# Optimization experiments

Measured on AMD Instinct MI355X. Metric: run time of the kernel, lower is better.

Reference implementation:

```python
import jax, jax.numpy as jnp
import numpy as np

H_DIM = 4096
N_HEADS = 4
D_HEAD = H_DIM // N_HEADS  # 1024; also forced to equal the node count N
N = D_HEAD
LN_EPS = 1e-5


def setup_inputs() -> dict:
    key = jax.random.key(0)
    ks = jax.random.split(key, 10)
    s = 0.02
    return {
        "node1": jax.random.normal(ks[0], (N, H_DIM), dtype=jnp.float32),
        "node2": jax.random.normal(ks[1], (N, H_DIM), dtype=jnp.float32),
        # stacked per-head projection weights (torch Linear y = x @ W^T + b; here W stored as [h, in, out])
        "Wq": jax.random.normal(ks[2], (N_HEADS, H_DIM, D_HEAD), dtype=jnp.float32) * s,
        "bq": jax.random.normal(ks[3], (N_HEADS, D_HEAD), dtype=jnp.float32) * s,
        "Wk": jax.random.normal(ks[4], (N_HEADS, H_DIM, D_HEAD), dtype=jnp.float32) * s,
        "bk": jax.random.normal(ks[5], (N_HEADS, D_HEAD), dtype=jnp.float32) * s,
        "Wv": jax.random.normal(ks[6], (N_HEADS, H_DIM, D_HEAD), dtype=jnp.float32) * s,
        "bv": jax.random.normal(ks[7], (N_HEADS, D_HEAD), dtype=jnp.float32) * s,
        "gamma": jnp.ones((H_DIM,), dtype=jnp.float32),
        "beta": jnp.zeros((H_DIM,), dtype=jnp.float32),
    }


def reference(node1, node2, Wq, bq, Wk, bk, Wv, bv, gamma, beta):
    # per-head projections: [h, N, d]
    q = jnp.einsum('nd,hdf->hnf', node1, Wq) + bq[:, None, :]
    k = jnp.einsum('md,hdf->hmf', node2, Wk) + bk[:, None, :]
    v = jnp.einsum('md,hdf->hmf', node2, Wv) + bv[:, None, :]
    scale = 1.0 / jnp.sqrt(jnp.asarray(D_HEAD, dtype=q.dtype))
    # scores [h, N, N]; elementwise-multiplied by v (no softmax). Valid because N == D_HEAD.
    r = (jnp.einsum('hnf,hmf->hnm', q, k) * scale) * v
    # concat heads along last dim: [N, h * d] = [N, H_DIM]
    out = jnp.transpose(r, (1, 0, 2)).reshape(N, H_DIM)
    # LayerNorm over last dim (biased variance, matching torch)
    mu = jnp.mean(out, axis=-1, keepdims=True)
    var = jnp.mean((out - mu) ** 2, axis=-1, keepdims=True)
    return (out - mu) * jax.lax.rsqrt(var + LN_EPS) * gamma + beta
```

## Files before the change

kernel.cpp:

```cpp
#include <hip/hip_runtime.h>

#define H_DIM 4096
#define DH 1024
#define NROWS 1024

typedef __attribute__((ext_vector_type(8))) short short8;
typedef __attribute__((ext_vector_type(4))) short short4v;
typedef __attribute__((ext_vector_type(4))) float f32x4;

#define AS_GLOBAL __attribute__((address_space(1)))
#define AS_LDS __attribute__((address_space(3)))

__device__ __forceinline__ short f2bf(float f) {
  union { float f; unsigned u; } v; v.f = f;
  unsigned r = v.u + 0x7fffu + ((v.u >> 16) & 1u);
  return (short)(r >> 16);
}
__device__ __forceinline__ float bf2f(short s) {
  union { unsigned u; float f; } v;
  v.u = ((unsigned)(unsigned short)s) << 16;
  return v.f;
}

__device__ __forceinline__ void gload16(const void* g, void* l) {
  __builtin_amdgcn_global_load_lds((const AS_GLOBAL void*)g, (AS_LDS void*)l, 16, 0, 0);
}

__global__ void convert_nodes(const float* __restrict__ n1, const float* __restrict__ n2,
                              short* __restrict__ o1, short* __restrict__ o2) {
  const float* src = blockIdx.y ? n2 : n1;
  short* dst = blockIdx.y ? o2 : o1;
  const size_t i = ((size_t)blockIdx.x * 256 + threadIdx.x) * 8;
  f32x4 a = *(const f32x4*)&src[i];
  f32x4 b = *(const f32x4*)&src[i + 4];
  short8 s;
  s[0] = f2bf(a.x); s[1] = f2bf(a.y); s[2] = f2bf(a.z); s[3] = f2bf(a.w);
  s[4] = f2bf(b.x); s[5] = f2bf(b.y); s[6] = f2bf(b.z); s[7] = f2bf(b.w);
  *(short8*)&dst[i] = s;
}

__global__ void convert_w_all(const float* __restrict__ Wq, const float* __restrict__ Wk,
                              const float* __restrict__ Wv, short* __restrict__ Wt) {
  __shared__ short tile[64][72];
  const int z = blockIdx.z, dt = blockIdx.y, ft = blockIdx.x;
  const float* W = (z < 4) ? Wq : (z < 8) ? Wk : Wv;
  const int h = z & 3;
  const float* Wh = W + (size_t)h * H_DIM * DH;
  short* Wth = Wt + (size_t)z * DH * H_DIM;
  const int t = threadIdx.x;
  {
    const int d = t >> 2, f0 = (t & 3) * 16;
    const float* src = Wh + (size_t)(dt * 64 + d) * DH + ft * 64 + f0;
    f32x4 v0 = *(const f32x4*)(src + 0);
    f32x4 v1 = *(const f32x4*)(src + 4);
    f32x4 v2 = *(const f32x4*)(src + 8);
    f32x4 v3 = *(const f32x4*)(src + 12);
    short8 s0, s1;
    s0[0] = f2bf(v0.x); s0[1] = f2bf(v0.y); s0[2] = f2bf(v0.z); s0[3] = f2bf(v0.w);
    s0[4] = f2bf(v1.x); s0[5] = f2bf(v1.y); s0[6] = f2bf(v1.z); s0[7] = f2bf(v1.w);
    s1[0] = f2bf(v2.x); s1[1] = f2bf(v2.y); s1[2] = f2bf(v2.z); s1[3] = f2bf(v2.w);
    s1[4] = f2bf(v3.x); s1[5] = f2bf(v3.y); s1[6] = f2bf(v3.z); s1[7] = f2bf(v3.w);
    *(short8*)&tile[d][f0] = s0;
    *(short8*)&tile[d][f0 + 8] = s1;
  }
  __syncthreads();
  {
    const int f = t >> 2, d0 = (t & 3) * 16;
    short8 o0, o1;
#pragma unroll
    for (int j = 0; j < 8; ++j) o0[j] = tile[d0 + j][f];
#pragma unroll
    for (int j = 0; j < 8; ++j) o1[j] = tile[d0 + 8 + j][f];
    short* dst = Wth + (size_t)(ft * 64 + f) * H_DIM + dt * 64 + d0;
    *(short8*)(dst) = o0;
    *(short8*)(dst + 8) = o1;
  }
}

#define BAR __builtin_amdgcn_s_barrier();
#define WAITL { asm volatile("s_waitcnt lgkmcnt(0)" ::: "memory"); __builtin_amdgcn_sched_barrier(0); }
#define WAITL4 { asm volatile("s_waitcnt lgkmcnt(4)" ::: "memory"); __builtin_amdgcn_sched_barrier(0); }
#define PRIO1 __builtin_amdgcn_s_setprio(1);
#define PRIO0 __builtin_amdgcn_s_setprio(0);

#define STG(isA, slab, ktn) \
  gload16(((isA) ? Ag : Bg) + (size_t)(slab) * 64 * H_DIM + (ktn) * 64, \
          smb + ((isA) ? 0 : 65536) + ((ktn) & 1) * 32768 + (slab) * 8192 + wub)

#define DSA(mh, cbuf) { _Pragma("unroll") for (int mp = 0; mp < 4; ++mp) { \
    const int rrow = wm * 128 + (mh) * 64 + mp * 16 + lr; \
    const char* pb = smb + (cbuf) * 32768 + rrow * 128; \
    af[mp * 2 + 0] = *(const short8*)(pb + sA0); \
    af[mp * 2 + 1] = *(const short8*)(pb + sA1); } }

#define DSB(nh, cbuf, dst) { _Pragma("unroll") for (int np = 0; np < 2; ++np) { \
    const int brow = wn * 64 + (nh) * 32 + np * 16 + lr; \
    const char* pb = smb + 65536 + (cbuf) * 32768 + brow * 128; \
    dst[np * 2 + 0] = *(const short8*)(pb + sA0); \
    dst[np * 2 + 1] = *(const short8*)(pb + sA1); } }

#define MFMA16(mh, nh, bfr) { _Pragma("unroll") for (int mp = 0; mp < 4; ++mp) \
    { _Pragma("unroll") for (int np = 0; np < 2; ++np) { \
      acc[(mh) * 4 + mp][(nh) * 2 + np] = __builtin_amdgcn_mfma_f32_16x16x32_bf16( \
          af[mp * 2 + 0], bfr[np * 2 + 0], acc[(mh) * 4 + mp][(nh) * 2 + np], 0, 0, 0); \
      acc[(mh) * 4 + mp][(nh) * 2 + np] = __builtin_amdgcn_mfma_f32_16x16x32_bf16( \
          af[mp * 2 + 1], bfr[np * 2 + 1], acc[(mh) * 4 + mp][(nh) * 2 + np], 0, 0, 0); } } }

__launch_bounds__(512, 2)
__global__ void qkv_8p(const short* __restrict__ n1b, const short* __restrict__ n2b,
                       const short* __restrict__ Wt,
                       const float* __restrict__ bq, const float* __restrict__ bk,
                       const float* __restrict__ bv,
                       short* __restrict__ qkv_out) {
  __shared__ short smem[65536];
  char* smb = (char*)smem;

  const int bid = blockIdx.x;
  const int v = (bid & 7) * 24 + (bid >> 3);
  const int gemm = v >> 4;
  const int rr = v & 15;
  const int mt = rr & 3, nt = rr >> 2;
  const int bm0 = mt * 256, bn0 = nt * 256;
  const short* A = (gemm < 4) ? n1b : n2b;
  const short* B = Wt + ((size_t)gemm << 22);
  const float* bias = ((gemm < 4) ? bq : (gemm < 8) ? bk : bv) + (gemm & 3) * DH;
  short* C = qkv_out + ((size_t)gemm << 20);

  const int t = threadIdx.x;
  const int lane = t & 63, w = t >> 6;
  const int wm = w >> 2, wn = w & 3;
  const int lr = lane & 15, lk = lane >> 4;
  const int xorv = lr & 7;
  const int sA0 = (lk ^ xorv) * 16;
  const int sA1 = ((4 + lk) ^ xorv) * 16;

  const int rowA = t >> 3;
  const int sL = (t & 7) ^ (rowA & 7);
  const size_t wub = (size_t)w * 1024;
  const short* Ag = A + (size_t)(bm0 + rowA) * H_DIM + sL * 8;
  const short* Bg = B + (size_t)(bn0 + rowA) * H_DIM + sL * 8;

  f32x4 acc[8][4];
#pragma unroll
  for (int m = 0; m < 8; ++m)
#pragma unroll
    for (int n = 0; n < 4; ++n)
      acc[m][n] = (f32x4)(0.0f);

  short8 af[8], bf0[4], bf1[4];

#pragma unroll
  for (int i = 0; i < 4; ++i) { STG(1, i, 0); }
#pragma unroll
  for (int i = 0; i < 4; ++i) { STG(0, i, 0); }
#pragma unroll
  for (int i = 0; i < 4; ++i) { STG(1, i, 1); }
#pragma unroll
  for (int i = 0; i < 4; ++i) { STG(0, i, 1); }
  asm volatile("s_waitcnt vmcnt(8)" ::: "memory");
  BAR

  const int NKT = H_DIM / 64;
  for (int kt = 0; kt < NKT; ++kt) {
    const int cb = kt & 1;
    const int dost = (kt + 2 < NKT);
    DSA(0, cb)
    DSB(0, cb, bf0)
    DSB(1, cb, bf1)
    WAITL4
    PRIO1 MFMA16(0, 0, bf0) PRIO0
    BAR
    if (dost) { STG(1, 0, kt + 2); STG(1, 2, kt + 2); }
    WAITL
    PRIO1 MFMA16(0, 1, bf1) PRIO0
    BAR
    DSA(1, cb)
    if (dost) { STG(0, 0, kt + 2); STG(0, 1, kt + 2); }
    WAITL
    PRIO1 MFMA16(1, 1, bf1) PRIO0
    BAR
    if (dost) { STG(0, 2, kt + 2); STG(0, 3, kt + 2); STG(1, 1, kt + 2); STG(1, 3, kt + 2); }
    PRIO1 MFMA16(1, 0, bf0) PRIO0
    if (dost)               { asm volatile("s_waitcnt vmcnt(8)" ::: "memory"); }
    else if (kt + 1 < NKT)  { asm volatile("s_waitcnt vmcnt(0)" ::: "memory"); }
    BAR
  }

  float bvv[4];
#pragma unroll
  for (int n = 0; n < 4; ++n) bvv[n] = bias[bn0 + wn * 64 + n * 16 + lr];
#pragma unroll
  for (int m = 0; m < 8; ++m) {
    const int row0 = bm0 + wm * 128 + m * 16 + lk * 4;
#pragma unroll
    for (int n = 0; n < 4; ++n) {
      const int col = bn0 + wn * 64 + n * 16 + lr;
#pragma unroll
      for (int e = 0; e < 4; ++e)
        C[(size_t)(row0 + e) * DH + col] = f2bf(acc[m][n][e] + bvv[n]);
    }
  }
}

__device__ __forceinline__ void stage_tile(const short* Xrow0, size_t rowstride, int kbase,
                                           short* lds, int t) {
  const int w = t >> 6;
#pragma unroll
  for (int p = 0; p < 2; ++p) {
    const short* g = Xrow0 + (size_t)(p * 64 + (t >> 2)) * rowstride + kbase + (t & 3) * 8;
    char* l = (char*)lds + p * 4096 + w * 1024;
    gload16(g, l);
  }
}

__launch_bounds__(256)
__global__ void attn_bt(const short* __restrict__ qkv, float* __restrict__ out) {
  const int bid = blockIdx.x;
  const int v = (bid & 7) * 32 + (bid >> 3);
  const int h = v >> 6;
  const int tile = v & 63;
  const short* Q = qkv + (size_t)h * NROWS * DH;
  const short* K = qkv + (size_t)(4 + h) * NROWS * DH;
  const short* V = qkv + (size_t)(8 + h) * NROWS * DH;
  const int bm0 = (tile >> 3) * 128, bn0 = (tile & 7) * 128;

  __shared__ short As[2][4096];
  __shared__ short Bs[2][4096];

  const int t = threadIdx.x;
  const int lane = t & 63, w = t >> 6;
  const int wm = (w >> 1) * 64, wn = (w & 1) * 64;
  const int lr = lane & 15, lk = lane >> 4;

  const short* Arow0 = Q + (size_t)bm0 * DH;
  const short* Brow0 = K + (size_t)bn0 * DH;

  f32x4 acc[4][4];
#pragma unroll
  for (int m = 0; m < 4; ++m)
#pragma unroll
    for (int n = 0; n < 4; ++n)
      acc[m][n] = (f32x4)(0.0f);

  stage_tile(Arow0, DH, 0, &As[0][0], t);
  stage_tile(Brow0, DH, 0, &Bs[0][0], t);
  __syncthreads();

  const int NKT = DH / 32;
  int cur = 0;
  for (int kt = 0; kt < NKT; ++kt) {
    if (kt + 1 < NKT) {
      stage_tile(Arow0, DH, (kt + 1) * 32, &As[cur ^ 1][0], t);
      stage_tile(Brow0, DH, (kt + 1) * 32, &Bs[cur ^ 1][0], t);
    }
    short8 af[4], bf_[4];
#pragma unroll
    for (int m = 0; m < 4; ++m)
      af[m] = *(const short8*)((const char*)&As[cur][0] + (wm + m * 16 + lr) * 64 + lk * 16);
#pragma unroll
    for (int n = 0; n < 4; ++n)
      bf_[n] = *(const short8*)((const char*)&Bs[cur][0] + (wn + n * 16 + lr) * 64 + lk * 16);
#pragma unroll
    for (int m = 0; m < 4; ++m)
#pragma unroll
      for (int n = 0; n < 4; ++n)
        acc[m][n] = __builtin_amdgcn_mfma_f32_16x16x32_bf16(af[m], bf_[n], acc[m][n], 0, 0, 0);
    __syncthreads();
    cur ^= 1;
  }

  const float scale = 0.03125f;
#pragma unroll
  for (int n = 0; n < 4; ++n) {
    const int col = bn0 + wn + n * 16 + lr;
#pragma unroll
    for (int m = 0; m < 4; ++m) {
      const int row0 = bm0 + wm + m * 16 + lk * 4;
#pragma unroll
      for (int r = 0; r < 4; ++r) {
        const int row = row0 + r;
        const float vv = bf2f(V[(size_t)row * DH + col]);
        out[(size_t)row * H_DIM + h * DH + col] = acc[m][n][r] * scale * vv;
      }
    }
  }
}

__launch_bounds__(256, 2)
__global__ void qkv_gemm(const float* __restrict__ node1,
                         const float* __restrict__ node2,
                         const float* __restrict__ Wq, const float* __restrict__ bq,
                         const float* __restrict__ Wk, const float* __restrict__ bk,
                         const float* __restrict__ Wv, const float* __restrict__ bv,
                         short* __restrict__ qkv_out) {
  const int gid = blockIdx.x;
  const int gemm = gid >> 6;
  const int tile = gid & 63;
  const int qkv = gemm >> 2;
  const int h = gemm & 3;
  const float* A = (qkv == 0) ? node1 : node2;
  const float* W = (qkv == 0) ? Wq : (qkv == 1 ? Wk : Wv);
  const float* bias = (qkv == 0) ? bq : (qkv == 1 ? bk : bv);
  const float* B = W + (size_t)h * H_DIM * DH;
  const float* bh = bias + h * DH;
  short* C = qkv_out + (size_t)gemm * NROWS * DH;
  const int bm0 = (tile >> 3) * 128;
  const int bn0 = (tile & 7) * 128;
  __shared__ short As[128][40];
  __shared__ short Bs[128][40];
  const int t = threadIdx.x;
  const int lane = t & 63;
  const int w = t >> 6;
  const int wm = (w >> 1) * 64;
  const int wn = (w & 1) * 64;
  const int lr = lane & 15;
  const int lk = lane >> 4;
  const int ar = t >> 3;
  const int ac = (t & 7) * 4;
  const int bfcX = t & 127;
  const int bd = (t >> 7) * 16;
  f32x4 acc[4][4];
#pragma unroll
  for (int m = 0; m < 4; ++m)
#pragma unroll
    for (int n = 0; n < 4; ++n)
      acc[m][n] = (f32x4)(0.0f);
  f32x4 rA[4];
  float rB[16];
  const float* Abase = A + (size_t)bm0 * H_DIM;
  const float* Bbase = B + bn0 + bfcX;
#pragma unroll
  for (int p = 0; p < 4; ++p)
    rA[p] = *(const f32x4*)&Abase[(size_t)(ar + 32 * p) * H_DIM + ac];
#pragma unroll
  for (int i = 0; i < 16; ++i)
    rB[i] = Bbase[(size_t)(bd + i) * DH];
  const int NKT = H_DIM / 32;
  for (int kt = 0; kt < NKT; ++kt) {
    __syncthreads();
#pragma unroll
    for (int p = 0; p < 4; ++p) {
      short4v s;
      s.x = f2bf(rA[p].x); s.y = f2bf(rA[p].y);
      s.z = f2bf(rA[p].z); s.w = f2bf(rA[p].w);
      *(short4v*)&As[ar + 32 * p][ac] = s;
    }
    {
      short8 lo, hi;
#pragma unroll
      for (int i = 0; i < 8; ++i) { lo[i] = f2bf(rB[i]); hi[i] = f2bf(rB[8 + i]); }
      *(short8*)&Bs[bfcX][bd] = lo;
      *(short8*)&Bs[bfcX][bd + 8] = hi;
    }
    __syncthreads();
    if (kt + 1 < NKT) {
      const int k0 = (kt + 1) * 32;
#pragma unroll
      for (int p = 0; p < 4; ++p)
        rA[p] = *(const f32x4*)&Abase[(size_t)(ar + 32 * p) * H_DIM + k0 + ac];
#pragma unroll
      for (int i = 0; i < 16; ++i)
        rB[i] = Bbase[(size_t)(k0 + bd + i) * DH];
    }
    short8 af[4], bf_[4];
#pragma unroll
    for (int m = 0; m < 4; ++m)
      af[m] = *(const short8*)&As[wm + m * 16 + lr][lk * 8];
#pragma unroll
    for (int n = 0; n < 4; ++n)
      bf_[n] = *(const short8*)&Bs[wn + n * 16 + lr][lk * 8];
#pragma unroll
    for (int m = 0; m < 4; ++m)
#pragma unroll
      for (int n = 0; n < 4; ++n)
        acc[m][n] = __builtin_amdgcn_mfma_f32_16x16x32_bf16(af[m], bf_[n], acc[m][n], 0, 0, 0);
  }
#pragma unroll
  for (int n = 0; n < 4; ++n) {
    const int col = bn0 + wn + n * 16 + lr;
    const float bv_ = bh[col];
#pragma unroll
    for (int m = 0; m < 4; ++m) {
      const int row0 = bm0 + wm + m * 16 + lk * 4;
#pragma unroll
      for (int r = 0; r < 4; ++r)
        C[(size_t)(row0 + r) * DH + col] = f2bf(acc[m][n][r] + bv_);
    }
  }
}

__launch_bounds__(256, 4)
__global__ void ln_kernel(float* __restrict__ out, const float* __restrict__ gamma,
                          const float* __restrict__ beta) {
  const int row = blockIdx.x;
  const int t = threadIdx.x;
  float* p = out + (size_t)row * H_DIM;
  f32x4 x[4];
  float s1 = 0.f, s2 = 0.f;
#pragma unroll
  for (int i = 0; i < 4; ++i) {
    x[i] = *(const f32x4*)&p[t * 4 + i * 1024];
    s1 += x[i].x + x[i].y + x[i].z + x[i].w;
    s2 += x[i].x * x[i].x + x[i].y * x[i].y + x[i].z * x[i].z + x[i].w * x[i].w;
  }
#pragma unroll
  for (int o = 32; o > 0; o >>= 1) {
    s1 += __shfl_down(s1, o);
    s2 += __shfl_down(s2, o);
  }
  __shared__ float w1[4], w2[4];
  if ((t & 63) == 0) { w1[t >> 6] = s1; w2[t >> 6] = s2; }
  __syncthreads();
  const float tot1 = w1[0] + w1[1] + w1[2] + w1[3];
  const float tot2 = w2[0] + w2[1] + w2[2] + w2[3];
  const float mu = tot1 * (1.0f / H_DIM);
  const float var = tot2 * (1.0f / H_DIM) - mu * mu;
  const float rs = rsqrtf(var + 1e-5f);
#pragma unroll
  for (int i = 0; i < 4; ++i) {
    const int c = t * 4 + i * 1024;
    const f32x4 g = *(const f32x4*)&gamma[c];
    const f32x4 b = *(const f32x4*)&beta[c];
    f32x4 y;
    y.x = (x[i].x - mu) * rs * g.x + b.x;
    y.y = (x[i].y - mu) * rs * g.y + b.y;
    y.z = (x[i].z - mu) * rs * g.z + b.z;
    y.w = (x[i].w - mu) * rs * g.w + b.w;
    *(f32x4*)&p[c] = y;
  }
}

extern "C" void kernel_launch(void* const* d_in, const int* in_sizes, int n_in,
                              void* d_out, int out_size, void* d_ws, size_t ws_size,
                              hipStream_t stream) {
  const float* node1 = (const float*)d_in[0];
  const float* node2 = (const float*)d_in[1];
  const float* Wq = (const float*)d_in[2];
  const float* bq = (const float*)d_in[3];
  const float* Wk = (const float*)d_in[4];
  const float* bk = (const float*)d_in[5];
  const float* Wv = (const float*)d_in[6];
  const float* bv = (const float*)d_in[7];
  const float* gamma = (const float*)d_in[8];
  const float* beta = (const float*)d_in[9];
  float* out = (float*)d_out;

  const size_t MB = (size_t)1 << 20;
  short* qkv = (short*)d_ws;
  short* n1b = qkv + ((size_t)12 << 20);
  short* n2b = n1b + ((size_t)4 << 20);
  short* Wt = qkv + ((size_t)20 << 20);

  if (ws_size >= 136 * MB) {
    convert_nodes<<<dim3(2048, 2), 256, 0, stream>>>(node1, node2, n1b, n2b);
    convert_w_all<<<dim3(16, 64, 12), 256, 0, stream>>>(Wq, Wk, Wv, Wt);
    qkv_8p<<<192, 512, 0, stream>>>(n1b, n2b, Wt, bq, bk, bv, qkv);
  } else {
    qkv_gemm<<<768, 256, 0, stream>>>(node1, node2, Wq, bq, Wk, bk, Wv, bv, qkv);
  }

  attn_bt<<<256, 256, 0, stream>>>(qkv, out);
  ln_kernel<<<1024, 256, 0, stream>>>(out, gamma, beta);
}
```

Baseline: 195.7 us.

## Double-buffer A fragments and regroup GEMM main loop into fewer barrier phases

The QKV projection GEMM main loop now loads both halves of the A fragments into separate register arrays up front, instead of reloading one array mid-iteration. The per-iteration schedule drops from four barrier-separated phases to three, and the global-to-LDS staging loads are regrouped into two batches. The aim is fewer barriers and more LDS-read latency hidden behind MFMA work. In exchange it uses 8 more short8 registers per thread, which under launch bounds of 512 threads and 2 blocks could cause register pressure or spills.

```diff
diff --git a/kernel.cpp b/kernel.cpp
--- a/kernel.cpp
+++ b/kernel.cpp
@@ -78,8 +78,9 @@
 }
 
 #define BAR __builtin_amdgcn_s_barrier();
+#define SGB0 __builtin_amdgcn_sched_barrier(0);
 #define WAITL { asm volatile("s_waitcnt lgkmcnt(0)" ::: "memory"); __builtin_amdgcn_sched_barrier(0); }
-#define WAITL4 { asm volatile("s_waitcnt lgkmcnt(4)" ::: "memory"); __builtin_amdgcn_sched_barrier(0); }
+#define WAITL8 { asm volatile("s_waitcnt lgkmcnt(8)" ::: "memory"); __builtin_amdgcn_sched_barrier(0); }
 #define PRIO1 __builtin_amdgcn_s_setprio(1);
 #define PRIO0 __builtin_amdgcn_s_setprio(0);
 
@@ -87,11 +88,11 @@
   gload16(((isA) ? Ag : Bg) + (size_t)(slab) * 64 * H_DIM + (ktn) * 64, \
           smb + ((isA) ? 0 : 65536) + ((ktn) & 1) * 32768 + (slab) * 8192 + wub)
 
-#define DSA(mh, cbuf) { _Pragma("unroll") for (int mp = 0; mp < 4; ++mp) { \
+#define DSA(dst, mh, cbuf) { _Pragma("unroll") for (int mp = 0; mp < 4; ++mp) { \
     const int rrow = wm * 128 + (mh) * 64 + mp * 16 + lr; \
     const char* pb = smb + (cbuf) * 32768 + rrow * 128; \
-    af[mp * 2 + 0] = *(const short8*)(pb + sA0); \
-    af[mp * 2 + 1] = *(const short8*)(pb + sA1); } }
+    dst[mp * 2 + 0] = *(const short8*)(pb + sA0); \
+    dst[mp * 2 + 1] = *(const short8*)(pb + sA1); } }
 
 #define DSB(nh, cbuf, dst) { _Pragma("unroll") for (int np = 0; np < 2; ++np) { \
     const int brow = wn * 64 + (nh) * 32 + np * 16 + lr; \
@@ -99,12 +100,12 @@
     dst[np * 2 + 0] = *(const short8*)(pb + sA0); \
     dst[np * 2 + 1] = *(const short8*)(pb + sA1); } }
 
-#define MFMA16(mh, nh, bfr) { _Pragma("unroll") for (int mp = 0; mp < 4; ++mp) \
+#define MFMA16(afr, mh, nh, bfr) { _Pragma("unroll") for (int mp = 0; mp < 4; ++mp) \
     { _Pragma("unroll") for (int np = 0; np < 2; ++np) { \
       acc[(mh) * 4 + mp][(nh) * 2 + np] = __builtin_amdgcn_mfma_f32_16x16x32_bf16( \
-          af[mp * 2 + 0], bfr[np * 2 + 0], acc[(mh) * 4 + mp][(nh) * 2 + np], 0, 0, 0); \
+          afr[mp * 2 + 0], bfr[np * 2 + 0], acc[(mh) * 4 + mp][(nh) * 2 + np], 0, 0, 0); \
       acc[(mh) * 4 + mp][(nh) * 2 + np] = __builtin_amdgcn_mfma_f32_16x16x32_bf16( \
-          af[mp * 2 + 1], bfr[np * 2 + 1], acc[(mh) * 4 + mp][(nh) * 2 + np], 0, 0, 0); } } }
+          afr[mp * 2 + 1], bfr[np * 2 + 1], acc[(mh) * 4 + mp][(nh) * 2 + np], 0, 0, 0); } } }
 
 __launch_bounds__(512, 2)
 __global__ void qkv_8p(const short* __restrict__ n1b, const short* __restrict__ n2b,
@@ -147,7 +148,7 @@
     for (int n = 0; n < 4; ++n)
       acc[m][n] = (f32x4)(0.0f);
 
-  short8 af[8], bf0[4], bf1[4];
+  short8 afA[8], afB[8], bf0[4], bf1[4];
 
 #pragma unroll
   for (int i = 0; i < 4; ++i) { STG(1, i, 0); }
@@ -164,23 +165,20 @@
   for (int kt = 0; kt < NKT; ++kt) {
     const int cb = kt & 1;
     const int dost = (kt + 2 < NKT);
-    DSA(0, cb)
+    DSA(afA, 0, cb)
     DSB(0, cb, bf0)
     DSB(1, cb, bf1)
-    WAITL4
-    PRIO1 MFMA16(0, 0, bf0) PRIO0
+    SGB0
+    DSA(afB, 1, cb)
+    WAITL8
+    PRIO1 MFMA16(afA, 0, 0, bf0) PRIO0
     BAR
-    if (dost) { STG(1, 0, kt + 2); STG(1, 2, kt + 2); }
+    if (dost) { STG(1, 0, kt + 2); STG(1, 2, kt + 2); STG(0, 0, kt + 2); STG(0, 1, kt + 2); }
+    PRIO1 MFMA16(afA, 0, 1, bf1) PRIO0
     WAITL
-    PRIO1 MFMA16(0, 1, bf1) PRIO0
     BAR
-    DSA(1, cb)
-    if (dost) { STG(0, 0, kt + 2); STG(0, 1, kt + 2); }
-    WAITL
-    PRIO1 MFMA16(1, 1, bf1) PRIO0
-    BAR
-    if (dost) { STG(0, 2, kt + 2); STG(0, 3, kt + 2); STG(1, 1, kt + 2); STG(1, 3, kt + 2); }
-    PRIO1 MFMA16(1, 0, bf0) PRIO0
+    if (dost) { STG(1, 1, kt + 2); STG(1, 3, kt + 2); STG(0, 2, kt + 2); STG(0, 3, kt + 2); }
+    PRIO1 MFMA16(afB, 1, 1, bf1) MFMA16(afB, 1, 0, bf0) PRIO0
     if (dost)               { asm volatile("s_waitcnt vmcnt(8)" ::: "memory"); }
     else if (kt + 1 < NKT)  { asm volatile("s_waitcnt vmcnt(0)" ::: "memory"); }
     BAR
```

New measurement: 200.3 us. +2.3%, slower.

## Store pre-LayerNorm intermediate as bf16 and merge conversion kernels

Applied to the files above, without the earlier changes.

Attention epilogue now writes the scaled product as bf16 into a workspace buffer instead of fp32 into the output, and the LayerNorm kernel reads bf16 and writes fp32 output. This cuts intermediate memory traffic roughly in half. Node and weight conversion kernels are merged into a single launch to drop one kernel launch. Risks added precision loss before LayerNorm.

```diff
diff --git a/kernel.cpp b/kernel.cpp
--- a/kernel.cpp
+++ b/kernel.cpp
@@ -26,28 +26,36 @@
   __builtin_amdgcn_global_load_lds((const AS_GLOBAL void*)g, (AS_LDS void*)l, 16, 0, 0);
 }
 
-__global__ void convert_nodes(const float* __restrict__ n1, const float* __restrict__ n2,
-                              short* __restrict__ o1, short* __restrict__ o2) {
-  const float* src = blockIdx.y ? n2 : n1;
-  short* dst = blockIdx.y ? o2 : o1;
-  const size_t i = ((size_t)blockIdx.x * 256 + threadIdx.x) * 8;
-  f32x4 a = *(const f32x4*)&src[i];
-  f32x4 b = *(const f32x4*)&src[i + 4];
-  short8 s;
-  s[0] = f2bf(a.x); s[1] = f2bf(a.y); s[2] = f2bf(a.z); s[3] = f2bf(a.w);
-  s[4] = f2bf(b.x); s[5] = f2bf(b.y); s[6] = f2bf(b.z); s[7] = f2bf(b.w);
-  *(short8*)&dst[i] = s;
-}
-
-__global__ void convert_w_all(const float* __restrict__ Wq, const float* __restrict__ Wk,
-                              const float* __restrict__ Wv, short* __restrict__ Wt) {
+__global__ void convert_all(const float* __restrict__ Wq, const float* __restrict__ Wk,
+                            const float* __restrict__ Wv,
+                            const float* __restrict__ n1, const float* __restrict__ n2,
+                            short* __restrict__ Wt, short* __restrict__ o1,
+                            short* __restrict__ o2) {
+  const int z = blockIdx.z;
+  const int t = threadIdx.x;
+  if (z == 12) {
+    const int b = blockIdx.y * 16 + blockIdx.x;
+    const float* src = (b < 512) ? n1 : n2;
+    short* dst = (b < 512) ? o1 : o2;
+    const size_t base = (size_t)(b & 511) * 8192;
+#pragma unroll
+    for (int it = 0; it < 4; ++it) {
+      const size_t i = base + it * 2048 + t * 8;
+      f32x4 a = *(const f32x4*)&src[i];
+      f32x4 c = *(const f32x4*)&src[i + 4];
+      short8 s;
+      s[0] = f2bf(a.x); s[1] = f2bf(a.y); s[2] = f2bf(a.z); s[3] = f2bf(a.w);
+      s[4] = f2bf(c.x); s[5] = f2bf(c.y); s[6] = f2bf(c.z); s[7] = f2bf(c.w);
+      *(short8*)&dst[i] = s;
+    }
+    return;
+  }
   __shared__ short tile[64][72];
-  const int z = blockIdx.z, dt = blockIdx.y, ft = blockIdx.x;
+  const int dt = blockIdx.y, ft = blockIdx.x;
   const float* W = (z < 4) ? Wq : (z < 8) ? Wk : Wv;
   const int h = z & 3;
   const float* Wh = W + (size_t)h * H_DIM * DH;
   short* Wth = Wt + (size_t)z * DH * H_DIM;
-  const int t = threadIdx.x;
   {
     const int d = t >> 2, f0 = (t & 3) * 16;
     const float* src = Wh + (size_t)(dt * 64 + d) * DH + ft * 64 + f0;
@@ -66,14 +74,14 @@
   __syncthreads();
   {
     const int f = t >> 2, d0 = (t & 3) * 16;
-    short8 o0, o1;
+    short8 o0, o1v;
 #pragma unroll
     for (int j = 0; j < 8; ++j) o0[j] = tile[d0 + j][f];
 #pragma unroll
-    for (int j = 0; j < 8; ++j) o1[j] = tile[d0 + 8 + j][f];
+    for (int j = 0; j < 8; ++j) o1v[j] = tile[d0 + 8 + j][f];
     short* dst = Wth + (size_t)(ft * 64 + f) * H_DIM + dt * 64 + d0;
     *(short8*)(dst) = o0;
-    *(short8*)(dst + 8) = o1;
+    *(short8*)(dst + 8) = o1v;
   }
 }
 
@@ -214,7 +222,7 @@
 }
 
 __launch_bounds__(256)
-__global__ void attn_bt(const short* __restrict__ qkv, float* __restrict__ out) {
+__global__ void attn_bt(const short* __restrict__ qkv, short* __restrict__ preln) {
   const int bid = blockIdx.x;
   const int v = (bid & 7) * 32 + (bid >> 3);
   const int h = v >> 6;
@@ -280,7 +288,7 @@
       for (int r = 0; r < 4; ++r) {
         const int row = row0 + r;
         const float vv = bf2f(V[(size_t)row * DH + col]);
-        out[(size_t)row * H_DIM + h * DH + col] = acc[m][n][r] * scale * vv;
+        preln[(size_t)row * H_DIM + h * DH + col] = f2bf(acc[m][n][r] * scale * vv);
       }
     }
   }
@@ -390,18 +398,22 @@
 }
 
 __launch_bounds__(256, 4)
-__global__ void ln_kernel(float* __restrict__ out, const float* __restrict__ gamma,
-                          const float* __restrict__ beta) {
+__global__ void ln_kernel(const short* __restrict__ preln, float* __restrict__ out,
+                          const float* __restrict__ gamma, const float* __restrict__ beta) {
   const int row = blockIdx.x;
   const int t = threadIdx.x;
-  float* p = out + (size_t)row * H_DIM;
-  f32x4 x[4];
+  const short* p = preln + (size_t)row * H_DIM;
+  float x[16];
   float s1 = 0.f, s2 = 0.f;
 #pragma unroll
-  for (int i = 0; i < 4; ++i) {
-    x[i] = *(const f32x4*)&p[t * 4 + i * 1024];
-    s1 += x[i].x + x[i].y + x[i].z + x[i].w;
-    s2 += x[i].x * x[i].x + x[i].y * x[i].y + x[i].z * x[i].z + x[i].w * x[i].w;
+  for (int i = 0; i < 2; ++i) {
+    short8 v = *(const short8*)&p[t * 8 + i * 2048];
+#pragma unroll
+    for (int j = 0; j < 8; ++j) {
+      const float f = bf2f(v[j]);
+      x[i * 8 + j] = f;
+      s1 += f; s2 += f * f;
+    }
   }
 #pragma unroll
   for (int o = 32; o > 0; o >>= 1) {
@@ -416,17 +428,25 @@
   const float mu = tot1 * (1.0f / H_DIM);
   const float var = tot2 * (1.0f / H_DIM) - mu * mu;
   const float rs = rsqrtf(var + 1e-5f);
-#pragma unroll
-  for (int i = 0; i < 4; ++i) {
-    const int c = t * 4 + i * 1024;
-    const f32x4 g = *(const f32x4*)&gamma[c];
-    const f32x4 b = *(const f32x4*)&beta[c];
-    f32x4 y;
-    y.x = (x[i].x - mu) * rs * g.x + b.x;
-    y.y = (x[i].y - mu) * rs * g.y + b.y;
-    y.z = (x[i].z - mu) * rs * g.z + b.z;
-    y.w = (x[i].w - mu) * rs * g.w + b.w;
-    *(f32x4*)&p[c] = y;
+  float* po = out + (size_t)row * H_DIM;
+#pragma unroll
+  for (int i = 0; i < 2; ++i) {
+    const int c = t * 8 + i * 2048;
+    const f32x4 g0 = *(const f32x4*)&gamma[c];
+    const f32x4 g1 = *(const f32x4*)&gamma[c + 4];
+    const f32x4 b0 = *(const f32x4*)&beta[c];
+    const f32x4 b1 = *(const f32x4*)&beta[c + 4];
+    f32x4 y0, y1;
+    y0.x = (x[i * 8 + 0] - mu) * rs * g0.x + b0.x;
+    y0.y = (x[i * 8 + 1] - mu) * rs * g0.y + b0.y;
+    y0.z = (x[i * 8 + 2] - mu) * rs * g0.z + b0.z;
+    y0.w = (x[i * 8 + 3] - mu) * rs * g0.w + b0.w;
+    y1.x = (x[i * 8 + 4] - mu) * rs * g1.x + b1.x;
+    y1.y = (x[i * 8 + 5] - mu) * rs * g1.y + b1.y;
+    y1.z = (x[i * 8 + 6] - mu) * rs * g1.z + b1.z;
+    y1.w = (x[i * 8 + 7] - mu) * rs * g1.w + b1.w;
+    *(f32x4*)&po[c] = y0;
+    *(f32x4*)&po[c + 4] = y1;
   }
 }
 
@@ -450,15 +470,16 @@
   short* n1b = qkv + ((size_t)12 << 20);
   short* n2b = n1b + ((size_t)4 << 20);
   short* Wt = qkv + ((size_t)20 << 20);
+  short* preln = n1b;
 
   if (ws_size >= 136 * MB) {
-    convert_nodes<<<dim3(2048, 2), 256, 0, stream>>>(node1, node2, n1b, n2b);
-    convert_w_all<<<dim3(16, 64, 12), 256, 0, stream>>>(Wq, Wk, Wv, Wt);
+    convert_all<<<dim3(16, 64, 13), 256, 0, stream>>>(Wq, Wk, Wv, node1, node2,
+                                                      Wt, n1b, n2b);
     qkv_8p<<<192, 512, 0, stream>>>(n1b, n2b, Wt, bq, bk, bv, qkv);
   } else {
     qkv_gemm<<<768, 256, 0, stream>>>(node1, node2, Wq, bq, Wk, bk, Wv, bv, qkv);
   }
 
-  attn_bt<<<256, 256, 0, stream>>>(qkv, out);
-  ln_kernel<<<1024, 256, 0, stream>>>(out, gamma, beta);
-}
+  attn_bt<<<256, 256, 0, stream>>>(qkv, preln);
+  ln_kernel<<<1024, 256, 0, stream>>>(preln, out, gamma, beta);
+}
```

Measured after the change: 191.8 us. -2.0%, faster.
